# Kernel tuning notes

Measured on AMD Instinct MI355X. Metric: run time of the kernel, lower is better.

The kernel has to match this reference:

```python
import math
import jax, jax.numpy as jnp
import numpy as np

D_MODEL = 1024
N_HEADS = 16
D_HEAD = D_MODEL // N_HEADS
BLOCK = 2048
BATCH = 2
SEQ = 2048


def setup_inputs() -> dict:
    key = jax.random.key(0)
    k1, k2, k3 = jax.random.split(key, 3)
    x = jax.random.normal(k1, (BATCH, SEQ, D_MODEL), dtype=jnp.float32)
    Wqkv = jax.random.normal(k2, (3 * D_MODEL, D_MODEL), dtype=jnp.float32) * 0.02
    Wo = jax.random.normal(k3, (D_MODEL, D_MODEL), dtype=jnp.float32) * 0.02
    # xi_init defaults to block/2
    log_xi = jnp.full((N_HEADS,), math.log(BLOCK / 2.0), dtype=jnp.float32)
    pi_gate_logit = jnp.full((N_HEADS,), 2.0, dtype=jnp.float32)
    e_gate_logit = jnp.full((N_HEADS,), 2.0, dtype=jnp.float32)
    return {"x": x, "Wqkv": Wqkv, "Wo": Wo, "log_xi": log_xi,
            "pi_gate_logit": pi_gate_logit, "e_gate_logit": e_gate_logit}


def _rotate(t, cos, sin):
    # t: (b, H, n, dh); cos/sin: (H, n, dh//2)
    t1 = t[..., 0::2]
    t2 = t[..., 1::2]
    r1 = t1 * cos - t2 * sin
    r2 = t1 * sin + t2 * cos
    # re-interleave even/odd lanes
    return jnp.stack([r1, r2], axis=-1).reshape(t.shape)


def reference(x, Wqkv, Wo, log_xi, pi_gate_logit, e_gate_logit):
    b, n, d = x.shape
    H, dh = N_HEADS, D_HEAD
    qkv = (x @ Wqkv.T).reshape(b, n, 3, H, dh)
    q = jnp.transpose(qkv[:, :, 0], (0, 2, 1, 3))  # (b,H,n,dh)
    k = jnp.transpose(qkv[:, :, 1], (0, 2, 1, 3))
    v = jnp.transpose(qkv[:, :, 2], (0, 2, 1, 3))

    pi_g = jax.nn.sigmoid(pi_gate_logit)  # (H,)
    e_g = jax.nn.sigmoid(e_gate_logit)    # (H,)

    kfrac = jnp.arange(0, dh, 2, dtype=jnp.float32) / dh
    pi_inv_freq = jnp.float32(math.pi) ** (1.0 - kfrac)  # (dh//2,)
    pos = jnp.arange(n, dtype=jnp.float32)
    theta = pos[:, None] * pi_inv_freq[None, :]           # (n, dh//2)
    theta = theta[None, :, :] * pi_g[:, None, None]       # (H, n, dh//2)
    cos, sin = jnp.cos(theta), jnp.sin(theta)

    q_rot = _rotate(q, cos, sin)
    k_rot = _rotate(k, cos, sin)

    scores = jnp.einsum('bhqd,bhkd->bhqk', q_rot, k_rot) / jnp.float32(math.sqrt(dh))

    xi = jnp.exp(log_xi)  # (H,)
    i = jnp.arange(n, dtype=jnp.float32)
    d_mat = jnp.abs(i[:, None] - i[None, :])              # (n, n)
    decay_bias = -(d_mat[None, :, :] / xi[:, None, None]) * e_g[:, None, None]  # (H,n,n)
    scores = scores + decay_bias[None]

    causal = jnp.tril(jnp.ones((n, n), dtype=bool))
    scores = jnp.where(causal[None, None], scores, jnp.float32(-jnp.inf))
    attn = jax.nn.softmax(scores, axis=-1)

    out = jnp.einsum('bhqk,bhkd->bhqd', attn, v)
    out = jnp.transpose(out, (0, 2, 1, 3)).reshape(b, n, d)
    return out @ Wo.T
```

## Files before the change

### kernel.cpp

```cpp
#include <hip/hip_runtime.h>

typedef unsigned short u16;
typedef unsigned int u32;
typedef __bf16 bf16x8 __attribute__((ext_vector_type(8)));
typedef float f32x4 __attribute__((ext_vector_type(4)));
typedef u16 u16x4 __attribute__((ext_vector_type(4)));

#define S_LEN 2048
#define NH 16
#define DH 64
#define DM 1024

#define GLDS(gp, lp) __builtin_amdgcn_global_load_lds( \
    (const __attribute__((address_space(1))) void*)(gp), \
    (__attribute__((address_space(3))) void*)(lp), 16, 0, 0)

__device__ __forceinline__ u16 f2bf(float f) {
  unsigned u = __float_as_uint(f);
  u += 0x7FFFu + ((u >> 16) & 1u);
  return (u16)(u >> 16);
}
__device__ __forceinline__ float bf2f(u16 h) {
  return __uint_as_float(((unsigned)h) << 16);
}

__global__ __launch_bounds__(256) void conv3_kernel(const float* __restrict__ a,
                                                    const float* __restrict__ wb,
                                                    const float* __restrict__ wc,
                                                    u16* __restrict__ oa,
                                                    u16* __restrict__ ob,
                                                    u16* __restrict__ oc) {
  int bid = blockIdx.x;
  const float* in;
  u16* out;
  int idx;
  if (bid < 2048)      { in = a;  out = oa; idx = bid; }
  else if (bid < 3584) { in = wb; out = ob; idx = bid - 2048; }
  else                 { in = wc; out = oc; idx = bid - 3584; }
  int i = idx * 2048 + threadIdx.x * 8;
  float4 v0 = *(const float4*)(in + i);
  float4 v1 = *(const float4*)(in + i + 4);
  u16x4 o0, o1;
  o0.x = f2bf(v0.x); o0.y = f2bf(v0.y); o0.z = f2bf(v0.z); o0.w = f2bf(v0.w);
  o1.x = f2bf(v1.x); o1.y = f2bf(v1.y); o1.z = f2bf(v1.z); o1.w = f2bf(v1.w);
  *(u16x4*)(out + i) = o0;
  *(u16x4*)(out + i + 4) = o1;
}

template <int OUTF32>
__global__ __launch_bounds__(256) void gemm_bt(const u16* __restrict__ A,
                                               const u16* __restrict__ B,
                                               void* __restrict__ C,
                                               int N, int K) {
  __shared__ __align__(16) u16 smem[16384];
  int tid = threadIdx.x;
  int w = tid >> 6, l = tid & 63, lg = l >> 4, lr = l & 15;
  int m0 = blockIdx.y * 128, n0 = blockIdx.x * 128;
  int wm = (w >> 1) * 64, wn = (w & 1) * 64;
  int NK = K >> 5;

  int srow0 = w * 16 + (l >> 2);
  int srow1 = srow0 + 64;
  int scol = (l & 3) * 8;
  const u16* gA0 = A + (size_t)(m0 + srow0) * K + scol;
  const u16* gA1 = A + (size_t)(m0 + srow1) * K + scol;
  const u16* gB0 = B + (size_t)(n0 + srow0) * K + scol;
  const u16* gB1 = B + (size_t)(n0 + srow1) * K + scol;

  auto stage = [&](int p) {
    u16* ab = smem + p * 8192;
    u16* bb = ab + 4096;
    GLDS(gA0, ab + w * 512);
    GLDS(gA1, ab + (4 + w) * 512);
    GLDS(gB0, bb + w * 512);
    GLDS(gB1, bb + (4 + w) * 512);
  };
  auto adv = [&]() { gA0 += 32; gA1 += 32; gB0 += 32; gB1 += 32; };

  f32x4 zero4 = {0.f, 0.f, 0.f, 0.f};
  f32x4 acc[4][4];
#pragma unroll
  for (int mt = 0; mt < 4; ++mt)
#pragma unroll
    for (int nt = 0; nt < 4; ++nt) acc[mt][nt] = zero4;

  stage(0);
  adv();
  __syncthreads();

  int p = 0;
  for (int kt = 0; kt < NK; ++kt) {
    bool pre = (kt + 1 < NK);
    if (pre) { stage(p ^ 1); adv(); }

    const u16* ab = smem + p * 8192;
    const u16* bb = ab + 4096;
    bf16x8 af[4], bfr[4];
#pragma unroll
    for (int mt = 0; mt < 4; ++mt)
      af[mt] = *(const bf16x8*)(ab + (wm + mt * 16 + lr) * 32 + lg * 8);
#pragma unroll
    for (int nt = 0; nt < 4; ++nt)
      bfr[nt] = *(const bf16x8*)(bb + (wn + nt * 16 + lr) * 32 + lg * 8);
    __builtin_amdgcn_s_setprio(1);
#pragma unroll
    for (int mt = 0; mt < 4; ++mt)
#pragma unroll
      for (int nt = 0; nt < 4; ++nt)
        acc[mt][nt] = __builtin_amdgcn_mfma_f32_16x16x32_bf16(af[mt], bfr[nt], acc[mt][nt], 0, 0, 0);
    __builtin_amdgcn_s_setprio(0);

    if (pre) {
      asm volatile("s_waitcnt vmcnt(0)" ::: "memory");
      __builtin_amdgcn_s_barrier();
    }
    p ^= 1;
  }

#pragma unroll
  for (int mt = 0; mt < 4; ++mt)
#pragma unroll
    for (int nt = 0; nt < 4; ++nt)
#pragma unroll
      for (int r = 0; r < 4; ++r) {
        int row = m0 + wm + mt * 16 + lg * 4 + r;
        int col = n0 + wn + nt * 16 + lr;
        float v = acc[mt][nt][r];
        if (OUTF32) ((float*)C)[(size_t)row * N + col] = v;
        else        ((u16*)C)[(size_t)row * N + col] = f2bf(v);
      }
}

__global__ __launch_bounds__(256) void rope_kernel(const u16* __restrict__ qkv,
                                                   const float* __restrict__ pi_gate_logit,
                                                   u16* __restrict__ qrot,
                                                   u16* __restrict__ krot,
                                                   u16* __restrict__ vt) {
  int st = blockIdx.x;
  int bh = blockIdx.y;
  int h = bh & 15;
  int t = threadIdx.x;
  int sl = t >> 2;
  int pb = t & 3;
  int d0 = pb * 16;
  int s = st * 64 + sl;
  int b = bh >> 4;
  size_t rowg = (size_t)(b * S_LEN + s) * (3 * DM) + h * DH + d0;

  float pg = 1.0f / (1.0f + __expf(-pi_gate_logit[h]));
  float spos = (float)s;
  float cs[8], sn[8];
#pragma unroll
  for (int j = 0; j < 8; ++j) {
    float p = (float)(pb * 8 + j);
    float fr = exp2f((1.0f - p * 0.03125f) * 1.6514961294723187f);
    float th = (spos * fr) * pg;
    float rev = th * 0.15915494309189535f;
    rev = rev - floorf(rev);
    cs[j] = __builtin_amdgcn_cosf(rev);
    sn[j] = __builtin_amdgcn_sinf(rev);
  }

#pragma unroll
  for (int which = 0; which < 2; ++which) {
    const u16* src = qkv + rowg + (size_t)which * DM;
    float sc = which ? 1.0f : 0.18033688011111772f;
    u16 in[16], ou[16];
    *(bf16x8*)(in)     = *(const bf16x8*)(src);
    *(bf16x8*)(in + 8) = *(const bf16x8*)(src + 8);
#pragma unroll
    for (int j = 0; j < 8; ++j) {
      float t1 = bf2f(in[2 * j]), t2 = bf2f(in[2 * j + 1]);
      ou[2 * j]     = f2bf((t1 * cs[j] - t2 * sn[j]) * sc);
      ou[2 * j + 1] = f2bf((t1 * sn[j] + t2 * cs[j]) * sc);
    }
    u16* dst = (which ? krot : qrot) + ((size_t)bh * S_LEN + s) * DH + d0;
    *(bf16x8*)(dst)     = *(bf16x8*)(ou);
    *(bf16x8*)(dst + 8) = *(bf16x8*)(ou + 8);
  }

  {
    const u16* src = qkv + rowg + 2 * DM;
    u16 in[16];
    *(bf16x8*)(in)     = *(const bf16x8*)(src);
    *(bf16x8*)(in + 8) = *(const bf16x8*)(src + 8);
#pragma unroll
    for (int e = 0; e < 16; ++e)
      vt[((size_t)bh * DH + d0 + e) * S_LEN + st * 64 + sl] = in[e];
  }
}

template <bool DIAG>
__device__ __forceinline__ void attn_tile(const unsigned char* __restrict__ kbuf,
                                          const unsigned char* __restrict__ vbuf,
                                          float mt, const float (&cbv)[16],
                                          const bf16x8 (&qf)[2],
                                          f32x4 (&oacc)[4],
                                          float& mrun, float& lrun,
                                          int lg, int lr, int il,
                                          unsigned char* pbuf) {
  f32x4 sacc[4];
#pragma unroll
  for (int nt = 0; nt < 4; ++nt)
#pragma unroll
    for (int r = 0; r < 4; ++r) sacc[nt][r] = cbv[nt * 4 + r] + mt;
  __builtin_amdgcn_s_setprio(1);
#pragma unroll
  for (int nt = 0; nt < 4; ++nt)
#pragma unroll
    for (int kk = 0; kk < 2; ++kk) {
      int row = nt * 16 + lr;
      int sl_ = lg + kk * 4;
      bf16x8 kf = *(const bf16x8*)(kbuf + row * 128 + ((sl_ ^ (row & 7)) << 4));
      sacc[nt] = __builtin_amdgcn_mfma_f32_16x16x32_bf16(kf, qf[kk], sacc[nt], 0, 0, 0);
    }
  __builtin_amdgcn_s_setprio(0);

  float pv[16];
#pragma unroll
  for (int nt = 0; nt < 4; ++nt)
#pragma unroll
    for (int r = 0; r < 4; ++r) {
      float v = sacc[nt][r];
      if (DIAG) {
        int jl = nt * 16 + lg * 4 + r;
        v = (jl <= il) ? v : -1e30f;
      }
      pv[nt * 4 + r] = v;
    }

  float m1 = pv[0];
#pragma unroll
  for (int i = 1; i < 16; ++i) m1 = fmaxf(m1, pv[i]);
  m1 = fmaxf(m1, __shfl_xor(m1, 16));
  m1 = fmaxf(m1, __shfl_xor(m1, 32));

  if (__ballot(m1 > 8.f)) {
    float d = fmaxf(m1, 0.f);
    float fac = __builtin_amdgcn_exp2f(-d);
    mrun += d;
    lrun *= fac;
    int fi = __float_as_int(fac);
    float facr[4];
#pragma unroll
    for (int r = 0; r < 4; ++r)
      facr[r] = __int_as_float(__builtin_amdgcn_ds_bpermute((4 * lg + r) << 2, fi));
#pragma unroll
    for (int nt = 0; nt < 4; ++nt)
#pragma unroll
      for (int r = 0; r < 4; ++r) oacc[nt][r] *= facr[r];
#pragma unroll
    for (int i = 0; i < 16; ++i) pv[i] -= d;
  }

  float p[16];
  float rsum = 0.f;
#pragma unroll
  for (int i = 0; i < 16; ++i) {
    p[i] = __builtin_amdgcn_exp2f(pv[i]);
    rsum += p[i];
  }
  rsum += __shfl_xor(rsum, 16);
  rsum += __shfl_xor(rsum, 32);
  lrun += rsum;

#pragma unroll
  for (int nt = 0; nt < 4; ++nt)
#pragma unroll
    for (int rp = 0; rp < 2; ++rp) {
      u32 pk;
      asm("v_cvt_pk_bf16_f32 %0, %1, %2" : "=v"(pk)
          : "v"(p[nt * 4 + 2 * rp]), "v"(p[nt * 4 + 2 * rp + 1]));
      *(u32*)(pbuf + ((lr * 128 + nt * 32 + lg * 8 + rp * 4) ^ ((lr & 7) << 4))) = pk;
    }
  asm volatile("s_waitcnt lgkmcnt(0)" ::: "memory");

  bf16x8 pf[2];
#pragma unroll
  for (int kk = 0; kk < 2; ++kk)
    pf[kk] = *(const bf16x8*)(pbuf + ((lr * 128 + (lg + 4 * kk) * 16) ^ ((lr & 7) << 4)));

  __builtin_amdgcn_s_setprio(1);
#pragma unroll
  for (int nt = 0; nt < 4; ++nt)
#pragma unroll
    for (int kk = 0; kk < 2; ++kk) {
      int row = nt * 16 + lr;
      int sl_ = lg + kk * 4;
      bf16x8 vf = *(const bf16x8*)(vbuf + row * 128 + ((sl_ ^ (row & 7)) << 4));
      oacc[nt] = __builtin_amdgcn_mfma_f32_16x16x32_bf16(pf[kk], vf, oacc[nt], 0, 0, 0);
    }
  __builtin_amdgcn_s_setprio(0);
}

__global__ __launch_bounds__(256, 3) void attn_kernel(const u16* __restrict__ qrot,
                                                      const u16* __restrict__ krot,
                                                      const u16* __restrict__ vt,
                                                      const float* __restrict__ log_xi,
                                                      const float* __restrict__ e_gate_logit,
                                                      u16* __restrict__ attnout) {
  int bh = blockIdx.x;
  int qt = 31 - blockIdx.y;
  int b = bh >> 4, h = bh & 15;
  int tid = threadIdx.x, w = tid >> 6, l = tid & 63, lg = l >> 4, lr = l & 15;
  int q0 = qt * 64;
  int il = w * 16 + lr;

  const float L2E = 1.4426950408889634f;
  float eg = 1.0f / (1.0f + __expf(-e_gate_logit[h]));
  float cdec2 = eg * __expf(-log_xi[h]) * L2E;

  __shared__ __align__(16) unsigned char smem[40960];
  unsigned char* pbuf = smem + 32768 + (w << 11);

  const size_t bhS = (size_t)bh * S_LEN;
  const u16* kb0 = krot + bhS * DH;
  const u16* vb0 = vt + (size_t)bh * DH * S_LEN;

  bf16x8 qf[2];
  {
    const u16* qp = qrot + (bhS + q0 + il) * DH + lg * 8;
    qf[0] = *(const bf16x8*)(qp);
    qf[1] = *(const bf16x8*)(qp + 32);
  }

  float cbv[16];
#pragma unroll
  for (int nt = 0; nt < 4; ++nt)
#pragma unroll
    for (int r = 0; r < 4; ++r)
      cbv[nt * 4 + r] = (float)(nt * 16 + lg * 4 + r) * cdec2;

  int c0 = tid, c1 = 256 + tid;
  int row0 = c0 >> 3, sl0 = c0 & 7;
  int row1 = c1 >> 3, sl1 = c1 & 7;

  bf16x8 kr[2], vr[2];
  auto load_kv = [&](int t) {
    kr[0] = *(const bf16x8*)(kb0 + (size_t)(t * 64 + row0) * DH + sl0 * 8);
    kr[1] = *(const bf16x8*)(kb0 + (size_t)(t * 64 + row1) * DH + sl1 * 8);
    vr[0] = *(const bf16x8*)(vb0 + (size_t)row0 * S_LEN + t * 64 + sl0 * 8);
    vr[1] = *(const bf16x8*)(vb0 + (size_t)row1 * S_LEN + t * 64 + sl1 * 8);
  };
  auto stage = [&](int p) {
    unsigned char* kb = smem + p * 8192;
    unsigned char* vb = smem + 16384 + p * 8192;
    *(bf16x8*)(kb + row0 * 128 + ((sl0 ^ (row0 & 7)) << 4)) = kr[0];
    *(bf16x8*)(kb + row1 * 128 + ((sl1 ^ (row1 & 7)) << 4)) = kr[1];
    *(bf16x8*)(vb + row0 * 128 + ((sl0 ^ (row0 & 7)) << 4)) = vr[0];
    *(bf16x8*)(vb + row1 * 128 + ((sl1 ^ (row1 & 7)) << 4)) = vr[1];
  };

  f32x4 zero4 = {0.f, 0.f, 0.f, 0.f};
  f32x4 oacc[4];
#pragma unroll
  for (int nt = 0; nt < 4; ++nt) oacc[nt] = zero4;
  float mrun = 0.f, lrun = 0.f;

  load_kv(0);
  float step = 64.f * cdec2;
  float tb = 0.f;
  int p = 0;
  for (int t = 0; t < qt; ++t, tb += step, p ^= 1) {
    stage(p);
    load_kv(t + 1);
    __syncthreads();
    attn_tile<false>(smem + p * 8192, smem + 16384 + p * 8192, tb - mrun, cbv,
                     qf, oacc, mrun, lrun, lg, lr, il, pbuf);
  }
  stage(p);
  __syncthreads();
  attn_tile<true>(smem + p * 8192, smem + 16384 + p * 8192, tb - mrun, cbv,
                  qf, oacc, mrun, lrun, lg, lr, il, pbuf);

  float lfin[4];
  int li = __float_as_int(lrun);
#pragma unroll
  for (int r = 0; r < 4; ++r)
    lfin[r] = __int_as_float(__builtin_amdgcn_ds_bpermute((4 * lg + r) << 2, li));
#pragma unroll
  for (int nt = 0; nt < 4; ++nt)
#pragma unroll
    for (int r = 0; r < 4; ++r) {
      int srow = q0 + w * 16 + lg * 4 + r;
      int col = h * DH + nt * 16 + lr;
      attnout[((size_t)b * S_LEN + srow) * DM + col] = f2bf(oacc[nt][r] / lfin[r]);
    }
}

extern "C" void kernel_launch(void* const* d_in, const int* in_sizes, int n_in,
                              void* d_out, int out_size, void* d_ws, size_t ws_size,
                              hipStream_t stream) {
  const float* x    = (const float*)d_in[0];
  const float* Wqkv = (const float*)d_in[1];
  const float* Wo   = (const float*)d_in[2];
  const float* log_xi        = (const float*)d_in[3];
  const float* pi_gate_logit = (const float*)d_in[4];
  const float* e_gate_logit  = (const float*)d_in[5];

  u16* xb     = (u16*)d_ws;
  u16* wqkvb  = xb + 4194304;
  u16* wob    = wqkvb + 3145728;
  u16* qkv    = wob + 1048576;
  u16* qrot   = qkv + 12582912;
  u16* krot   = qrot + 4194304;
  u16* vt     = krot + 4194304;
  u16* attno  = vt + 4194304;

  conv3_kernel<<<4096, 256, 0, stream>>>(x, Wqkv, Wo, xb, wqkvb, wob);

  gemm_bt<0><<<dim3(24, 32), 256, 0, stream>>>(xb, wqkvb, qkv, 3072, 1024);

  rope_kernel<<<dim3(32, 32), 256, 0, stream>>>(qkv, pi_gate_logit, qrot, krot, vt);

  attn_kernel<<<dim3(32, 32), 256, 0, stream>>>(qrot, krot, vt, log_xi, e_gate_logit, attno);

  gemm_bt<1><<<dim3(8, 32), 256, 0, stream>>>(attno, wob, d_out, 1024, 1024);
}
```

Baseline: 112.3 us.

## Process two query tiles per attention block to share K/V tile loads

Each attention workgroup now handles two adjacent 64-row query tiles (128 rows), reusing every staged K/V tile and its LDS fragment reads for both sets of MFMAs. The grid is halved in y, and the final diagonal tile for the lower query tile is skipped for the upper one. This halves global K/V traffic and LDS staging per query row and interleaves two independent softmax chains for ILP, at the cost of doubled accumulator registers, more LDS, and fewer workgroups, which may reduce occupancy under the 3-blocks launch bound.

```diff
diff --git a/kernel.cpp b/kernel.cpp
--- a/kernel.cpp
+++ b/kernel.cpp
@@ -10,6 +10,10 @@
 #define NH 16
 #define DH 64
 #define DM 1024
+
+#define M_FULL 0
+#define M_DIAG 1
+#define M_SKIP 2
 
 #define GLDS(gp, lp) __builtin_amdgcn_global_load_lds( \
     (const __attribute__((address_space(1))) void*)(gp), \
@@ -190,39 +194,18 @@
   }
 }
 
-template <bool DIAG>
-__device__ __forceinline__ void attn_tile(const unsigned char* __restrict__ kbuf,
-                                          const unsigned char* __restrict__ vbuf,
-                                          float mt, const float (&cbv)[16],
-                                          const bf16x8 (&qf)[2],
-                                          f32x4 (&oacc)[4],
-                                          float& mrun, float& lrun,
-                                          int lg, int lr, int il,
-                                          unsigned char* pbuf) {
-  f32x4 sacc[4];
-#pragma unroll
-  for (int nt = 0; nt < 4; ++nt)
-#pragma unroll
-    for (int r = 0; r < 4; ++r) sacc[nt][r] = cbv[nt * 4 + r] + mt;
-  __builtin_amdgcn_s_setprio(1);
-#pragma unroll
-  for (int nt = 0; nt < 4; ++nt)
-#pragma unroll
-    for (int kk = 0; kk < 2; ++kk) {
-      int row = nt * 16 + lr;
-      int sl_ = lg + kk * 4;
-      bf16x8 kf = *(const bf16x8*)(kbuf + row * 128 + ((sl_ ^ (row & 7)) << 4));
-      sacc[nt] = __builtin_amdgcn_mfma_f32_16x16x32_bf16(kf, qf[kk], sacc[nt], 0, 0, 0);
-    }
-  __builtin_amdgcn_s_setprio(0);
-
+template <int M>
+__device__ __forceinline__ void softmax_pack(f32x4 (&sacc)[4], f32x4 (&oacc)[4],
+                                             float& mrun, float& lrun,
+                                             int lg, int lr, int il,
+                                             unsigned char* pbuf) {
   float pv[16];
 #pragma unroll
   for (int nt = 0; nt < 4; ++nt)
 #pragma unroll
     for (int r = 0; r < 4; ++r) {
       float v = sacc[nt][r];
-      if (DIAG) {
+      if constexpr (M == M_DIAG) {
         int jl = nt * 16 + lg * 4 + r;
         v = (jl <= il) ? v : -1e30f;
       }
@@ -273,23 +256,74 @@
           : "v"(p[nt * 4 + 2 * rp]), "v"(p[nt * 4 + 2 * rp + 1]));
       *(u32*)(pbuf + ((lr * 128 + nt * 32 + lg * 8 + rp * 4) ^ ((lr & 7) << 4))) = pk;
     }
+}
+
+template <int MA, int MB>
+__device__ __forceinline__ void tile_dual(const unsigned char* __restrict__ kbuf,
+                                          const unsigned char* __restrict__ vbuf,
+                                          float mtA, float mtB, const float (&cbv)[16],
+                                          const bf16x8 (&qfA)[2], const bf16x8 (&qfB)[2],
+                                          f32x4 (&oaccA)[4], f32x4 (&oaccB)[4],
+                                          float& mrunA, float& lrunA,
+                                          float& mrunB, float& lrunB,
+                                          int lg, int lr, int il,
+                                          unsigned char* pbufA, unsigned char* pbufB) {
+  f32x4 saccA[4], saccB[4];
+  if constexpr (MA != M_SKIP) {
+#pragma unroll
+    for (int nt = 0; nt < 4; ++nt)
+#pragma unroll
+      for (int r = 0; r < 4; ++r) saccA[nt][r] = cbv[nt * 4 + r] + mtA;
+  }
+#pragma unroll
+  for (int nt = 0; nt < 4; ++nt)
+#pragma unroll
+    for (int r = 0; r < 4; ++r) saccB[nt][r] = cbv[nt * 4 + r] + mtB;
+
+  __builtin_amdgcn_s_setprio(1);
+#pragma unroll
+  for (int nt = 0; nt < 4; ++nt) {
+    int row = nt * 16 + lr;
+    bf16x8 kf0 = *(const bf16x8*)(kbuf + row * 128 + ((lg ^ (row & 7)) << 4));
+    bf16x8 kf1 = *(const bf16x8*)(kbuf + row * 128 + (((lg + 4) ^ (row & 7)) << 4));
+    if constexpr (MA != M_SKIP) {
+      saccA[nt] = __builtin_amdgcn_mfma_f32_16x16x32_bf16(kf0, qfA[0], saccA[nt], 0, 0, 0);
+      saccA[nt] = __builtin_amdgcn_mfma_f32_16x16x32_bf16(kf1, qfA[1], saccA[nt], 0, 0, 0);
+    }
+    saccB[nt] = __builtin_amdgcn_mfma_f32_16x16x32_bf16(kf0, qfB[0], saccB[nt], 0, 0, 0);
+    saccB[nt] = __builtin_amdgcn_mfma_f32_16x16x32_bf16(kf1, qfB[1], saccB[nt], 0, 0, 0);
+  }
+  __builtin_amdgcn_s_setprio(0);
+
+  if constexpr (MA != M_SKIP)
+    softmax_pack<MA>(saccA, oaccA, mrunA, lrunA, lg, lr, il, pbufA);
+  softmax_pack<MB>(saccB, oaccB, mrunB, lrunB, lg, lr, il, pbufB);
+
   asm volatile("s_waitcnt lgkmcnt(0)" ::: "memory");
 
-  bf16x8 pf[2];
+  bf16x8 pfA[2], pfB[2];
+  if constexpr (MA != M_SKIP) {
+#pragma unroll
+    for (int kk = 0; kk < 2; ++kk)
+      pfA[kk] = *(const bf16x8*)(pbufA + ((lr * 128 + (lg + 4 * kk) * 16) ^ ((lr & 7) << 4)));
+  }
 #pragma unroll
   for (int kk = 0; kk < 2; ++kk)
-    pf[kk] = *(const bf16x8*)(pbuf + ((lr * 128 + (lg + 4 * kk) * 16) ^ ((lr & 7) << 4)));
+    pfB[kk] = *(const bf16x8*)(pbufB + ((lr * 128 + (lg + 4 * kk) * 16) ^ ((lr & 7) << 4)));
 
   __builtin_amdgcn_s_setprio(1);
 #pragma unroll
-  for (int nt = 0; nt < 4; ++nt)
-#pragma unroll
-    for (int kk = 0; kk < 2; ++kk) {
-      int row = nt * 16 + lr;
-      int sl_ = lg + kk * 4;
-      bf16x8 vf = *(const bf16x8*)(vbuf + row * 128 + ((sl_ ^ (row & 7)) << 4));
-      oacc[nt] = __builtin_amdgcn_mfma_f32_16x16x32_bf16(pf[kk], vf, oacc[nt], 0, 0, 0);
-    }
+  for (int nt = 0; nt < 4; ++nt) {
+    int row = nt * 16 + lr;
+    bf16x8 vf0 = *(const bf16x8*)(vbuf + row * 128 + ((lg ^ (row & 7)) << 4));
+    bf16x8 vf1 = *(const bf16x8*)(vbuf + row * 128 + (((lg + 4) ^ (row & 7)) << 4));
+    if constexpr (MA != M_SKIP) {
+      oaccA[nt] = __builtin_amdgcn_mfma_f32_16x16x32_bf16(pfA[0], vf0, oaccA[nt], 0, 0, 0);
+      oaccA[nt] = __builtin_amdgcn_mfma_f32_16x16x32_bf16(pfA[1], vf1, oaccA[nt], 0, 0, 0);
+    }
+    oaccB[nt] = __builtin_amdgcn_mfma_f32_16x16x32_bf16(pfB[0], vf0, oaccB[nt], 0, 0, 0);
+    oaccB[nt] = __builtin_amdgcn_mfma_f32_16x16x32_bf16(pfB[1], vf1, oaccB[nt], 0, 0, 0);
+  }
   __builtin_amdgcn_s_setprio(0);
 }
 
@@ -300,28 +334,32 @@
                                                       const float* __restrict__ e_gate_logit,
                                                       u16* __restrict__ attnout) {
   int bh = blockIdx.x;
-  int qt = 31 - blockIdx.y;
+  int qp = 15 - blockIdx.y;
   int b = bh >> 4, h = bh & 15;
   int tid = threadIdx.x, w = tid >> 6, l = tid & 63, lg = l >> 4, lr = l & 15;
-  int q0 = qt * 64;
+  int Q0 = qp * 128;
   int il = w * 16 + lr;
 
   const float L2E = 1.4426950408889634f;
   float eg = 1.0f / (1.0f + __expf(-e_gate_logit[h]));
   float cdec2 = eg * __expf(-log_xi[h]) * L2E;
 
-  __shared__ __align__(16) unsigned char smem[40960];
-  unsigned char* pbuf = smem + 32768 + (w << 11);
+  __shared__ __align__(16) unsigned char smem[49152];
+  unsigned char* pbufA = smem + 32768 + (w << 11);
+  unsigned char* pbufB = smem + 40960 + (w << 11);
 
   const size_t bhS = (size_t)bh * S_LEN;
   const u16* kb0 = krot + bhS * DH;
   const u16* vb0 = vt + (size_t)bh * DH * S_LEN;
 
-  bf16x8 qf[2];
+  bf16x8 qfA[2], qfB[2];
   {
-    const u16* qp = qrot + (bhS + q0 + il) * DH + lg * 8;
-    qf[0] = *(const bf16x8*)(qp);
-    qf[1] = *(const bf16x8*)(qp + 32);
+    const u16* qpA = qrot + (bhS + Q0 + il) * DH + lg * 8;
+    qfA[0] = *(const bf16x8*)(qpA);
+    qfA[1] = *(const bf16x8*)(qpA + 32);
+    const u16* qpB = qpA + 64 * DH;
+    qfB[0] = *(const bf16x8*)(qpB);
+    qfB[1] = *(const bf16x8*)(qpB + 32);
   }
 
   float cbv[16];
@@ -352,40 +390,70 @@
   };
 
   f32x4 zero4 = {0.f, 0.f, 0.f, 0.f};
-  f32x4 oacc[4];
-#pragma unroll
-  for (int nt = 0; nt < 4; ++nt) oacc[nt] = zero4;
-  float mrun = 0.f, lrun = 0.f;
+  f32x4 oaccA[4], oaccB[4];
+#pragma unroll
+  for (int nt = 0; nt < 4; ++nt) { oaccA[nt] = zero4; oaccB[nt] = zero4; }
+  float mrunA = 0.f, lrunA = 0.f, mrunB = 0.f, lrunB = 0.f;
 
   load_kv(0);
   float step = 64.f * cdec2;
   float tb = 0.f;
   int p = 0;
-  for (int t = 0; t < qt; ++t, tb += step, p ^= 1) {
+  for (int t = 0; t < 2 * qp; ++t, tb += step, p ^= 1) {
     stage(p);
     load_kv(t + 1);
     __syncthreads();
-    attn_tile<false>(smem + p * 8192, smem + 16384 + p * 8192, tb - mrun, cbv,
-                     qf, oacc, mrun, lrun, lg, lr, il, pbuf);
-  }
+    tile_dual<M_FULL, M_FULL>(smem + p * 8192, smem + 16384 + p * 8192,
+                              tb - mrunA, tb - mrunB, cbv, qfA, qfB,
+                              oaccA, oaccB, mrunA, lrunA, mrunB, lrunB,
+                              lg, lr, il, pbufA, pbufB);
+  }
+  stage(p);
+  load_kv(2 * qp + 1);
+  __syncthreads();
+  tile_dual<M_DIAG, M_FULL>(smem + p * 8192, smem + 16384 + p * 8192,
+                            tb - mrunA, tb - mrunB, cbv, qfA, qfB,
+                            oaccA, oaccB, mrunA, lrunA, mrunB, lrunB,
+                            lg, lr, il, pbufA, pbufB);
+  tb += step;
+  p ^= 1;
   stage(p);
   __syncthreads();
-  attn_tile<true>(smem + p * 8192, smem + 16384 + p * 8192, tb - mrun, cbv,
-                  qf, oacc, mrun, lrun, lg, lr, il, pbuf);
-
-  float lfin[4];
-  int li = __float_as_int(lrun);
-#pragma unroll
-  for (int r = 0; r < 4; ++r)
-    lfin[r] = __int_as_float(__builtin_amdgcn_ds_bpermute((4 * lg + r) << 2, li));
-#pragma unroll
-  for (int nt = 0; nt < 4; ++nt)
-#pragma unroll
-    for (int r = 0; r < 4; ++r) {
-      int srow = q0 + w * 16 + lg * 4 + r;
-      int col = h * DH + nt * 16 + lr;
-      attnout[((size_t)b * S_LEN + srow) * DM + col] = f2bf(oacc[nt][r] / lfin[r]);
-    }
+  tile_dual<M_SKIP, M_DIAG>(smem + p * 8192, smem + 16384 + p * 8192,
+                            0.f, tb - mrunB, cbv, qfA, qfB,
+                            oaccA, oaccB, mrunA, lrunA, mrunB, lrunB,
+                            lg, lr, il, pbufA, pbufB);
+
+  {
+    float lfin[4];
+    int li = __float_as_int(lrunA);
+#pragma unroll
+    for (int r = 0; r < 4; ++r)
+      lfin[r] = __int_as_float(__builtin_amdgcn_ds_bpermute((4 * lg + r) << 2, li));
+#pragma unroll
+    for (int nt = 0; nt < 4; ++nt)
+#pragma unroll
+      for (int r = 0; r < 4; ++r) {
+        int srow = Q0 + w * 16 + lg * 4 + r;
+        int col = h * DH + nt * 16 + lr;
+        attnout[((size_t)b * S_LEN + srow) * DM + col] = f2bf(oaccA[nt][r] / lfin[r]);
+      }
+  }
+  {
+    float lfin[4];
+    int li = __float_as_int(lrunB);
+#pragma unroll
+    for (int r = 0; r < 4; ++r)
+      lfin[r] = __int_as_float(__builtin_amdgcn_ds_bpermute((4 * lg + r) << 2, li));
+#pragma unroll
+    for (int nt = 0; nt < 4; ++nt)
+#pragma unroll
+      for (int r = 0; r < 4; ++r) {
+        int srow = Q0 + 64 + w * 16 + lg * 4 + r;
+        int col = h * DH + nt * 16 + lr;
+        attnout[((size_t)b * S_LEN + srow) * DM + col] = f2bf(oaccB[nt][r] / lfin[r]);
+      }
+  }
 }
 
 extern "C" void kernel_launch(void* const* d_in, const int* in_sizes, int n_in,
@@ -413,7 +481,7 @@
 
   rope_kernel<<<dim3(32, 32), 256, 0, stream>>>(qkv, pi_gate_logit, qrot, krot, vt);
 
-  attn_kernel<<<dim3(32, 32), 256, 0, stream>>>(qrot, krot, vt, log_xi, e_gate_logit, attno);
+  attn_kernel<<<dim3(32, 16), 256, 0, stream>>>(qrot, krot, vt, log_xi, e_gate_logit, attno);
 
   gemm_bt<1><<<dim3(8, 32), 256, 0, stream>>>(attno, wob, d_out, 1024, 1024);
 }
```

Result: slower. 124.8 us (+11.1%).

## Fuse RoPE and V transpose into QKV GEMM epilogue

Applied to the files above, without the earlier changes.

Removes the separate rope kernel and the intermediate qkv buffer by applying the rotary rotation, q scaling and V transposition directly in the QKV GEMM's epilogue. Lane pairs exchange even/odd values via shuffles to rotate in registers. This avoids writing and rereading a 24MB bf16 qkv tensor and one launch, but adds transcendental math to the GEMM epilogue and uses scattered 2-byte stores for q/k.

```diff
diff --git a/kernel.cpp b/kernel.cpp
--- a/kernel.cpp
+++ b/kernel.cpp
@@ -47,11 +47,15 @@
   *(u16x4*)(out + i + 4) = o1;
 }
 
-template <int OUTF32>
+template <int MODE>
 __global__ __launch_bounds__(256) void gemm_bt(const u16* __restrict__ A,
                                                const u16* __restrict__ B,
                                                void* __restrict__ C,
-                                               int N, int K) {
+                                               int N, int K,
+                                               const float* __restrict__ pi_gate_logit,
+                                               u16* __restrict__ qrot,
+                                               u16* __restrict__ krot,
+                                               u16* __restrict__ vtp) {
   __shared__ __align__(16) u16 smem[16384];
   int tid = threadIdx.x;
   int w = tid >> 6, l = tid & 63, lg = l >> 4, lr = l & 15;
@@ -117,76 +121,67 @@
     p ^= 1;
   }
 
-#pragma unroll
-  for (int mt = 0; mt < 4; ++mt)
-#pragma unroll
-    for (int nt = 0; nt < 4; ++nt)
-#pragma unroll
-      for (int r = 0; r < 4; ++r) {
-        int row = m0 + wm + mt * 16 + lg * 4 + r;
-        int col = n0 + wn + nt * 16 + lr;
-        float v = acc[mt][nt][r];
-        if (OUTF32) ((float*)C)[(size_t)row * N + col] = v;
-        else        ((u16*)C)[(size_t)row * N + col] = f2bf(v);
+  if constexpr (MODE != 2) {
+#pragma unroll
+    for (int mt = 0; mt < 4; ++mt)
+#pragma unroll
+      for (int nt = 0; nt < 4; ++nt)
+#pragma unroll
+        for (int r = 0; r < 4; ++r) {
+          int row = m0 + wm + mt * 16 + lg * 4 + r;
+          int col = n0 + wn + nt * 16 + lr;
+          float v = acc[mt][nt][r];
+          if (MODE == 1) ((float*)C)[(size_t)row * N + col] = v;
+          else           ((u16*)C)[(size_t)row * N + col] = f2bf(v);
+        }
+  } else {
+    int region = n0 >> 10;
+    int hh = ((n0 + wn) >> 6) & 15;
+    if (region < 2) {
+      float pg = 1.0f / (1.0f + __expf(-pi_gate_logit[hh]));
+      float sc = region ? 1.0f : 0.18033688011111772f;
+      u16* dst = region ? krot : qrot;
+      float cfreq[4];
+#pragma unroll
+      for (int nt = 0; nt < 4; ++nt) {
+        float pp = (float)((nt * 16 + lr) >> 1);
+        cfreq[nt] = exp2f((1.0f - pp * 0.03125f) * 1.6514961294723187f) * pg;
       }
-}
-
-__global__ __launch_bounds__(256) void rope_kernel(const u16* __restrict__ qkv,
-                                                   const float* __restrict__ pi_gate_logit,
-                                                   u16* __restrict__ qrot,
-                                                   u16* __restrict__ krot,
-                                                   u16* __restrict__ vt) {
-  int st = blockIdx.x;
-  int bh = blockIdx.y;
-  int h = bh & 15;
-  int t = threadIdx.x;
-  int sl = t >> 2;
-  int pb = t & 3;
-  int d0 = pb * 16;
-  int s = st * 64 + sl;
-  int b = bh >> 4;
-  size_t rowg = (size_t)(b * S_LEN + s) * (3 * DM) + h * DH + d0;
-
-  float pg = 1.0f / (1.0f + __expf(-pi_gate_logit[h]));
-  float spos = (float)s;
-  float cs[8], sn[8];
-#pragma unroll
-  for (int j = 0; j < 8; ++j) {
-    float p = (float)(pb * 8 + j);
-    float fr = exp2f((1.0f - p * 0.03125f) * 1.6514961294723187f);
-    float th = (spos * fr) * pg;
-    float rev = th * 0.15915494309189535f;
-    rev = rev - floorf(rev);
-    cs[j] = __builtin_amdgcn_cosf(rev);
-    sn[j] = __builtin_amdgcn_sinf(rev);
-  }
-
-#pragma unroll
-  for (int which = 0; which < 2; ++which) {
-    const u16* src = qkv + rowg + (size_t)which * DM;
-    float sc = which ? 1.0f : 0.18033688011111772f;
-    u16 in[16], ou[16];
-    *(bf16x8*)(in)     = *(const bf16x8*)(src);
-    *(bf16x8*)(in + 8) = *(const bf16x8*)(src + 8);
-#pragma unroll
-    for (int j = 0; j < 8; ++j) {
-      float t1 = bf2f(in[2 * j]), t2 = bf2f(in[2 * j + 1]);
-      ou[2 * j]     = f2bf((t1 * cs[j] - t2 * sn[j]) * sc);
-      ou[2 * j + 1] = f2bf((t1 * sn[j] + t2 * cs[j]) * sc);
-    }
-    u16* dst = (which ? krot : qrot) + ((size_t)bh * S_LEN + s) * DH + d0;
-    *(bf16x8*)(dst)     = *(bf16x8*)(ou);
-    *(bf16x8*)(dst + 8) = *(bf16x8*)(ou + 8);
-  }
-
-  {
-    const u16* src = qkv + rowg + 2 * DM;
-    u16 in[16];
-    *(bf16x8*)(in)     = *(const bf16x8*)(src);
-    *(bf16x8*)(in + 8) = *(const bf16x8*)(src + 8);
-#pragma unroll
-    for (int e = 0; e < 16; ++e)
-      vt[((size_t)bh * DH + d0 + e) * S_LEN + st * 64 + sl] = in[e];
+#pragma unroll
+      for (int mt = 0; mt < 4; ++mt)
+#pragma unroll
+        for (int r = 0; r < 4; ++r) {
+          int row = m0 + wm + mt * 16 + lg * 4 + r;
+          int s = row & 2047, bb2 = row >> 11;
+          size_t base = ((size_t)((bb2 * 16 + hh) * 2048 + s)) * 64;
+          float fs = (float)s;
+#pragma unroll
+          for (int nt = 0; nt < 4; ++nt) {
+            float mine = acc[mt][nt][r];
+            float other = __shfl_xor(mine, 1);
+            float rev = fs * cfreq[nt] * 0.15915494309189535f;
+            rev -= floorf(rev);
+            float cs = __builtin_amdgcn_cosf(rev);
+            float sn = __builtin_amdgcn_sinf(rev);
+            float rot = (lr & 1) ? (other * sn + mine * cs)
+                                 : (mine * cs - other * sn);
+            dst[base + nt * 16 + lr] = f2bf(rot * sc);
+          }
+        }
+    } else {
+#pragma unroll
+      for (int mt = 0; mt < 4; ++mt)
+#pragma unroll
+        for (int nt = 0; nt < 4; ++nt) {
+          int row0r = m0 + wm + mt * 16 + lg * 4;
+          int s = row0r & 2047, bb2 = row0r >> 11;
+          int d = nt * 16 + lr;
+          u16x4 o;
+          o.x = f2bf(acc[mt][nt][0]); o.y = f2bf(acc[mt][nt][1]);
+          o.z = f2bf(acc[mt][nt][2]); o.w = f2bf(acc[mt][nt][3]);
+          *(u16x4*)(vtp + ((size_t)((bb2 * 16 + hh) * 64 + d)) * 2048 + s) = o;
+        }
+    }
   }
 }
 
@@ -401,19 +396,18 @@
   u16* xb     = (u16*)d_ws;
   u16* wqkvb  = xb + 4194304;
   u16* wob    = wqkvb + 3145728;
-  u16* qkv    = wob + 1048576;
-  u16* qrot   = qkv + 12582912;
+  u16* qrot   = wob + 1048576;
   u16* krot   = qrot + 4194304;
   u16* vt     = krot + 4194304;
   u16* attno  = vt + 4194304;
 
   conv3_kernel<<<4096, 256, 0, stream>>>(x, Wqkv, Wo, xb, wqkvb, wob);
 
-  gemm_bt<0><<<dim3(24, 32), 256, 0, stream>>>(xb, wqkvb, qkv, 3072, 1024);
-
-  rope_kernel<<<dim3(32, 32), 256, 0, stream>>>(qkv, pi_gate_logit, qrot, krot, vt);
+  gemm_bt<2><<<dim3(24, 32), 256, 0, stream>>>(xb, wqkvb, nullptr, 3072, 1024,
+                                               pi_gate_logit, qrot, krot, vt);
 
   attn_kernel<<<dim3(32, 32), 256, 0, stream>>>(qrot, krot, vt, log_xi, e_gate_logit, attno);
 
-  gemm_bt<1><<<dim3(8, 32), 256, 0, stream>>>(attno, wob, d_out, 1024, 1024);
-}
+  gemm_bt<1><<<dim3(8, 32), 256, 0, stream>>>(attno, wob, d_out, 1024, 1024,
+                                              nullptr, nullptr, nullptr, nullptr);
+}
```

Measured after the change: 104.8 us. 1.07x faster.
